# Kernel optimization log

Hardware: AMD Instinct MI355X
Metric: run time of the kernel (lower is better)

Reference implementation:

```python
import jax, jax.numpy as jnp
import numpy as np
import math

N, S, C, K, V = 32, 4096, 1, 512, 128
TARGET_SCALE = 0.06  # normalize_scale == embedding_scale when normalize=True


def setup_inputs() -> dict:
    key = jax.random.key(0)
    k1, k2 = jax.random.split(key)
    x0 = jax.random.normal(k1, (N, S, C, V), dtype=jnp.float32)
    emb = jax.random.normal(k2, (C, K, V), dtype=jnp.float32) * TARGET_SCALE
    # after_update(): renormalize each code vector to norm = embedding_scale*sqrt(V)
    tn = TARGET_SCALE * math.sqrt(V)
    emb = emb * (tn / jnp.linalg.norm(emb, axis=2, keepdims=True))
    return {"x0": x0, "embedding0": emb}


def _vq_forward(x0, embedding0):
    tn = TARGET_SCALE * math.sqrt(V)
    # normalize inputs and codebook to the same norm (normalize=True path)
    x = tn * x0 / jnp.linalg.norm(x0, axis=3, keepdims=True)              # (N,S,C,V)
    emb = tn * embedding0 / jnp.linalg.norm(embedding0, axis=2, keepdims=True)  # (C,K,V)

    xf = x.reshape(N * S, C, V)
    x2 = jnp.sum(xf * xf, axis=2)                     # (NS, C)
    e2 = jnp.sum(emb * emb, axis=2)                   # (C, K)
    dots = jnp.einsum('ncv,ckv->nck', xf, emb)        # (NS, C, K)
    d2 = x2[:, :, None] + e2[None, :, :] - 2.0 * dots
    index = jnp.argmin(d2, axis=2)                    # (NS, C) int

    # entropy of code usage: histc over n_classes, normalized by len(index)=NS
    hist = jnp.zeros((K,), jnp.float32).at[index.reshape(-1)].add(1.0)
    prob = hist / float(N * S)
    entropy = -jnp.sum(jnp.where(hist > 0, prob * jnp.log(jnp.where(hist > 0, prob, 1.0)), 0.0))

    # gather selected code vectors per channel
    output = emb[jnp.arange(C)[None, :], index]       # (NS, C, V)
    output = output.reshape(x.shape)                  # (N,S,C,V)

    sg = jax.lax.stop_gradient
    out0 = sg(output - x) + x                                              # straight-through
    out1 = jnp.sum((sg(x) - output) ** 2, axis=3)                          # codebook loss (N,S,C)
    out2 = jnp.sum((x - sg(output)) ** 2, axis=3) + jnp.sum((x - x0) ** 2, axis=3)  # commitment + norm penalty
    return out0, out1, out2, entropy


def reference(x0, embedding0):
    return _vq_forward(x0, embedding0)
```

## Files before the change

### kernel.cpp

```cpp
#include <hip/hip_runtime.h>
#include <math.h>

#define VDIM   128
#define KCODES 512
#define NROWS  (32 * 4096)
#define TILE_ROWS 512
#define NBLK (NROWS / TILE_ROWS)
#define TN 0.67882250993908565f

typedef __attribute__((ext_vector_type(8))) short bf16x8;
typedef __attribute__((ext_vector_type(4))) float f32x4;

__device__ __forceinline__ unsigned short f2bf(float f) {
    unsigned u = __float_as_uint(f);
    unsigned r = u + 0x7FFFu + ((u >> 16) & 1u);
    return (unsigned short)(r >> 16);
}

__device__ __forceinline__ bf16x8 pack8(f32x4 a, f32x4 b) {
    bf16x8 v;
    v[0] = (short)f2bf(a[0]); v[1] = (short)f2bf(a[1]);
    v[2] = (short)f2bf(a[2]); v[3] = (short)f2bf(a[3]);
    v[4] = (short)f2bf(b[0]); v[5] = (short)f2bf(b[1]);
    v[6] = (short)f2bf(b[2]); v[7] = (short)f2bf(b[3]);
    return v;
}

__global__ __launch_bounds__(1024, 1) void vq_fused(
        const float* __restrict__ x0,
        const float* __restrict__ emb0,
        unsigned short* __restrict__ hist_part,
        float* __restrict__ out0,
        float* __restrict__ out1,
        float* __restrict__ out2) {
    __shared__ uint4 sB[8192];
    __shared__ float sscale[KCODES];
    __shared__ int   shist[KCODES];
    __shared__ int   sbesti[TILE_ROWS];

    int t = threadIdx.x;
    int w = t >> 6;
    int l = t & 63;
    int n15 = l & 15;
    int q = l >> 4;

    int rowbase = blockIdx.x * TILE_ROWS + (w << 5);

    f32x4 ax[2][4][2];
    #pragma unroll
    for (int s = 0; s < 2; ++s) {
        const float* xrow = x0 + (size_t)(rowbase + (s << 4) + n15) * VDIM + (q << 3);
        #pragma unroll
        for (int kc = 0; kc < 4; ++kc) {
            const f32x4* xp = (const f32x4*)(xrow + (kc << 5));
            ax[s][kc][0] = xp[0];
            ax[s][kc][1] = xp[1];
        }
    }
    __builtin_amdgcn_sched_barrier(0);

    if (t < KCODES) shist[t] = 0;

    #pragma unroll 4
    for (int i = 0; i < 32; ++i) {
        int k = (w << 5) + i;
        const float* row = emb0 + (size_t)k * VDIM;
        float a = row[l];
        float b = row[l + 64];
        float ss = a * a + b * b;
        #pragma unroll
        for (int off = 32; off; off >>= 1) ss += __shfl_xor(ss, off);
        if (l == 0) sscale[k] = TN / sqrtf(ss);
    }

    __syncthreads();

    #pragma unroll
    for (int i = 0; i < 8; ++i) {
        int g = (i << 10) + t;
        int k = ((g >> 8) << 4) | (g & 15);
        int d0 = ((g >> 4) & 15) << 3;
        float s = sscale[k];
        const f32x4* ep = (const f32x4*)(emb0 + (size_t)k * VDIM + d0);
        f32x4 a = ep[0], b = ep[1];
        f32x4 as, bs;
        as[0] = a[0] * s; as[1] = a[1] * s; as[2] = a[2] * s; as[3] = a[3] * s;
        bs[0] = b[0] * s; bs[1] = b[1] * s; bs[2] = b[2] * s; bs[3] = b[3] * s;
        ((bf16x8*)sB)[g] = pack8(as, bs);
    }

    bf16x8 afr[2][4];
    float nsq[2];
    #pragma unroll
    for (int s = 0; s < 2; ++s) {
        float p0 = 0.f, p1 = 0.f;
        #pragma unroll
        for (int kc = 0; kc < 4; ++kc) {
            f32x4 a = ax[s][kc][0], b = ax[s][kc][1];
            p0 = fmaf(a[0], a[0], p0); p1 = fmaf(a[1], a[1], p1);
            p0 = fmaf(a[2], a[2], p0); p1 = fmaf(a[3], a[3], p1);
            p0 = fmaf(b[0], b[0], p0); p1 = fmaf(b[1], b[1], p1);
            p0 = fmaf(b[2], b[2], p0); p1 = fmaf(b[3], b[3], p1);
            afr[s][kc] = pack8(a, b);
        }
        nsq[s] = p0 + p1;
        nsq[s] += __shfl_xor(nsq[s], 16, 64);
        nsq[s] += __shfl_xor(nsq[s], 32, 64);
    }

    float best[2][4];
    int   bidx[2][4];
    #pragma unroll
    for (int s = 0; s < 2; ++s)
        #pragma unroll
        for (int r = 0; r < 4; ++r) { best[s][r] = -3.4e38f; bidx[s][r] = 0; }

    const f32x4 zero4 = {0.f, 0.f, 0.f, 0.f};

    __syncthreads();

    #pragma unroll 2
    for (int cn = 0; cn < 32; ++cn) {
        const bf16x8* bls = ((const bf16x8*)sB) + (cn << 8) + l;
        bf16x8 b0 = bls[0], b1 = bls[64], b2 = bls[128], b3 = bls[192];
        int nbase = (cn << 4) + n15;
        #pragma unroll
        for (int s = 0; s < 2; ++s) {
            f32x4 acc = __builtin_amdgcn_mfma_f32_16x16x32_bf16(afr[s][0], b0, zero4, 0, 0, 0);
            acc = __builtin_amdgcn_mfma_f32_16x16x32_bf16(afr[s][1], b1, acc, 0, 0, 0);
            acc = __builtin_amdgcn_mfma_f32_16x16x32_bf16(afr[s][2], b2, acc, 0, 0, 0);
            acc = __builtin_amdgcn_mfma_f32_16x16x32_bf16(afr[s][3], b3, acc, 0, 0, 0);
            #pragma unroll
            for (int r = 0; r < 4; ++r) {
                float d = acc[r];
                if (d > best[s][r]) { best[s][r] = d; bidx[s][r] = nbase; }
            }
        }
    }

    #pragma unroll
    for (int m = 1; m <= 8; m <<= 1) {
        #pragma unroll
        for (int s = 0; s < 2; ++s)
            #pragma unroll
            for (int r = 0; r < 4; ++r) {
                float ov = __shfl_xor(best[s][r], m, 64);
                int   oi = __shfl_xor(bidx[s][r], m, 64);
                if (ov > best[s][r] || (ov == best[s][r] && oi < bidx[s][r])) {
                    best[s][r] = ov; bidx[s][r] = oi;
                }
            }
    }

    int r3 = l & 3;
    bool own = (((l & 15) >> 2) == q);
    if (own) {
        #pragma unroll
        for (int s = 0; s < 2; ++s) {
            int rl = (s << 4) + (l & 15);
            size_t row = (size_t)rowbase + rl;
            float dv = best[s][r3];
            int   bv = bidx[s][r3];
            float nn = nsq[s];
            float sc = TN / sqrtf(nn);
            float o1 = 2.f * TN * TN - 2.f * sc * dv;
            __builtin_nontemporal_store(o1, &out1[row]);
            float sm = sc - 1.f;
            __builtin_nontemporal_store(o1 + sm * sm * nn, &out2[row]);
            atomicAdd(&shist[bv], 1);
            sbesti[(w << 5) + rl] = bv;
        }
    }

    #pragma unroll 4
    for (int p = 0; p < 16; ++p) {
        int rl = (p << 1) + (l >> 5);
        int bi = sbesti[(w << 5) + rl];
        float s = sscale[bi];
        int v4 = l & 31;
        f32x4 e = *((const f32x4*)(emb0 + (size_t)bi * VDIM) + v4);
        f32x4 o;
        o[0] = e[0] * s; o[1] = e[1] * s; o[2] = e[2] * s; o[3] = e[3] * s;
        __builtin_nontemporal_store(
            o, (f32x4*)(out0 + ((size_t)rowbase + rl) * (size_t)VDIM) + v4);
    }

    __syncthreads();

    if (t < KCODES)
        hist_part[((size_t)blockIdx.x << 9) + t] = (unsigned short)shist[t];
}

__global__ __launch_bounds__(1024) void entropy_k(
        const unsigned short* __restrict__ hp,
        float* __restrict__ out) {
    __shared__ int   s2[1024];
    __shared__ float red[8];
    int t = threadIdx.x;
    int c = t & 511;
    int half = t >> 9;
    int sum = 0;
    #pragma unroll 8
    for (int b = half * 128; b < half * 128 + 128; ++b)
        sum += hp[(b << 9) + c];
    s2[t] = sum;
    __syncthreads();
    if (t < 512) {
        float h = (float)(s2[t] + s2[t + 512]);
        float p = h / (float)NROWS;
        float term = (h > 0.f) ? p * logf(p) : 0.f;
        #pragma unroll
        for (int off = 32; off; off >>= 1) term += __shfl_xor(term, off);
        if ((t & 63) == 0) red[t >> 6] = term;
    }
    __syncthreads();
    if (t == 0) {
        float ssum = 0.f;
        #pragma unroll
        for (int i = 0; i < 8; i++) ssum += red[i];
        out[0] = -ssum;
    }
}

extern "C" void kernel_launch(void* const* d_in, const int* in_sizes, int n_in,
                              void* d_out, int out_size, void* d_ws, size_t ws_size,
                              hipStream_t stream) {
    const float* x0   = (const float*)d_in[0];
    const float* emb0 = (const float*)d_in[1];

    unsigned short* hist_part = (unsigned short*)d_ws;

    float* out  = (float*)d_out;
    float* out0 = out;
    float* out1 = out0 + (size_t)NROWS * VDIM;
    float* out2 = out1 + NROWS;
    float* oent = out2 + NROWS;

    vq_fused<<<NBLK, 1024, 0, stream>>>(x0, emb0, hist_part, out0, out1, out2);
    entropy_k<<<1, 1024, 0, stream>>>(hist_part, oent);
}
```

Before: 157.8 us.

## Halve row tile, stage codebook in two halves, use global atomic histogram

```diff
diff --git a/kernel.cpp b/kernel.cpp
--- a/kernel.cpp
+++ b/kernel.cpp
@@ -4,8 +4,9 @@
 #define VDIM   128
 #define KCODES 512
 #define NROWS  (32 * 4096)
-#define TILE_ROWS 512
+#define TILE_ROWS 256
 #define NBLK (NROWS / TILE_ROWS)
+#define STAGE_CODES 256
 #define TN 0.67882250993908565f
 
 typedef __attribute__((ext_vector_type(8))) short bf16x8;
@@ -26,14 +27,14 @@
     return v;
 }
 
-__global__ __launch_bounds__(1024, 1) void vq_fused(
+__global__ __launch_bounds__(1024, 8) void vq_fused(
         const float* __restrict__ x0,
         const float* __restrict__ emb0,
-        unsigned short* __restrict__ hist_part,
+        unsigned* __restrict__ hist,
         float* __restrict__ out0,
         float* __restrict__ out1,
         float* __restrict__ out2) {
-    __shared__ uint4 sB[8192];
+    __shared__ uint4 sB[4096];
     __shared__ float sscale[KCODES];
     __shared__ int   shist[KCODES];
     __shared__ int   sbesti[TILE_ROWS];
@@ -44,20 +45,18 @@
     int n15 = l & 15;
     int q = l >> 4;
 
-    int rowbase = blockIdx.x * TILE_ROWS + (w << 5);
-
-    f32x4 ax[2][4][2];
-    #pragma unroll
-    for (int s = 0; s < 2; ++s) {
-        const float* xrow = x0 + (size_t)(rowbase + (s << 4) + n15) * VDIM + (q << 3);
+    int rowbase = blockIdx.x * TILE_ROWS + (w << 4);
+
+    f32x4 ax[4][2];
+    {
+        const float* xrow = x0 + (size_t)(rowbase + n15) * VDIM + (q << 3);
         #pragma unroll
         for (int kc = 0; kc < 4; ++kc) {
             const f32x4* xp = (const f32x4*)(xrow + (kc << 5));
-            ax[s][kc][0] = xp[0];
-            ax[s][kc][1] = xp[1];
-        }
-    }
-    __builtin_amdgcn_sched_barrier(0);
+            ax[kc][0] = xp[0];
+            ax[kc][1] = xp[1];
+        }
+    }
 
     if (t < KCODES) shist[t] = 0;
 
@@ -75,65 +74,64 @@
 
     __syncthreads();
 
-    #pragma unroll
-    for (int i = 0; i < 8; ++i) {
-        int g = (i << 10) + t;
-        int k = ((g >> 8) << 4) | (g & 15);
-        int d0 = ((g >> 4) & 15) << 3;
-        float s = sscale[k];
-        const f32x4* ep = (const f32x4*)(emb0 + (size_t)k * VDIM + d0);
-        f32x4 a = ep[0], b = ep[1];
-        f32x4 as, bs;
-        as[0] = a[0] * s; as[1] = a[1] * s; as[2] = a[2] * s; as[3] = a[3] * s;
-        bs[0] = b[0] * s; bs[1] = b[1] * s; bs[2] = b[2] * s; bs[3] = b[3] * s;
-        ((bf16x8*)sB)[g] = pack8(as, bs);
-    }
-
-    bf16x8 afr[2][4];
-    float nsq[2];
-    #pragma unroll
-    for (int s = 0; s < 2; ++s) {
+    bf16x8 afr[4];
+    float nsq;
+    {
         float p0 = 0.f, p1 = 0.f;
         #pragma unroll
         for (int kc = 0; kc < 4; ++kc) {
-            f32x4 a = ax[s][kc][0], b = ax[s][kc][1];
+            f32x4 a = ax[kc][0], b = ax[kc][1];
             p0 = fmaf(a[0], a[0], p0); p1 = fmaf(a[1], a[1], p1);
             p0 = fmaf(a[2], a[2], p0); p1 = fmaf(a[3], a[3], p1);
             p0 = fmaf(b[0], b[0], p0); p1 = fmaf(b[1], b[1], p1);
             p0 = fmaf(b[2], b[2], p0); p1 = fmaf(b[3], b[3], p1);
-            afr[s][kc] = pack8(a, b);
-        }
-        nsq[s] = p0 + p1;
-        nsq[s] += __shfl_xor(nsq[s], 16, 64);
-        nsq[s] += __shfl_xor(nsq[s], 32, 64);
-    }
-
-    float best[2][4];
-    int   bidx[2][4];
+            afr[kc] = pack8(a, b);
+        }
+        nsq = p0 + p1;
+        nsq += __shfl_xor(nsq, 16, 64);
+        nsq += __shfl_xor(nsq, 32, 64);
+    }
+
+    float best[4];
+    int   bidx[4];
     #pragma unroll
-    for (int s = 0; s < 2; ++s)
-        #pragma unroll
-        for (int r = 0; r < 4; ++r) { best[s][r] = -3.4e38f; bidx[s][r] = 0; }
+    for (int r = 0; r < 4; ++r) { best[r] = -3.4e38f; bidx[r] = 0; }
 
     const f32x4 zero4 = {0.f, 0.f, 0.f, 0.f};
 
-    __syncthreads();
-
-    #pragma unroll 2
-    for (int cn = 0; cn < 32; ++cn) {
-        const bf16x8* bls = ((const bf16x8*)sB) + (cn << 8) + l;
-        bf16x8 b0 = bls[0], b1 = bls[64], b2 = bls[128], b3 = bls[192];
-        int nbase = (cn << 4) + n15;
-        #pragma unroll
-        for (int s = 0; s < 2; ++s) {
-            f32x4 acc = __builtin_amdgcn_mfma_f32_16x16x32_bf16(afr[s][0], b0, zero4, 0, 0, 0);
-            acc = __builtin_amdgcn_mfma_f32_16x16x32_bf16(afr[s][1], b1, acc, 0, 0, 0);
-            acc = __builtin_amdgcn_mfma_f32_16x16x32_bf16(afr[s][2], b2, acc, 0, 0, 0);
-            acc = __builtin_amdgcn_mfma_f32_16x16x32_bf16(afr[s][3], b3, acc, 0, 0, 0);
+    #pragma unroll 1
+    for (int st = 0; st < 2; ++st) {
+        if (st) __syncthreads();
+
+        int kofs = st << 8;
+        #pragma unroll
+        for (int i = 0; i < 4; ++i) {
+            int g = (i << 10) + t;
+            int k = kofs + (((g >> 8) << 4) | (g & 15));
+            int d0 = ((g >> 4) & 15) << 3;
+            float s = sscale[k];
+            const f32x4* ep = (const f32x4*)(emb0 + (size_t)k * VDIM + d0);
+            f32x4 a = ep[0], b = ep[1];
+            f32x4 as, bs;
+            as[0] = a[0] * s; as[1] = a[1] * s; as[2] = a[2] * s; as[3] = a[3] * s;
+            bs[0] = b[0] * s; bs[1] = b[1] * s; bs[2] = b[2] * s; bs[3] = b[3] * s;
+            ((bf16x8*)sB)[g] = pack8(as, bs);
+        }
+        __syncthreads();
+
+        #pragma unroll 2
+        for (int cn = 0; cn < 16; ++cn) {
+            const bf16x8* bls = ((const bf16x8*)sB) + (cn << 8) + l;
+            bf16x8 b0 = bls[0], b1 = bls[64], b2 = bls[128], b3 = bls[192];
+            int nbase = kofs + (cn << 4) + n15;
+            f32x4 acc = __builtin_amdgcn_mfma_f32_16x16x32_bf16(afr[0], b0, zero4, 0, 0, 0);
+            acc = __builtin_amdgcn_mfma_f32_16x16x32_bf16(afr[1], b1, acc, 0, 0, 0);
+            acc = __builtin_amdgcn_mfma_f32_16x16x32_bf16(afr[2], b2, acc, 0, 0, 0);
+            acc = __builtin_amdgcn_mfma_f32_16x16x32_bf16(afr[3], b3, acc, 0, 0, 0);
             #pragma unroll
             for (int r = 0; r < 4; ++r) {
                 float d = acc[r];
-                if (d > best[s][r]) { best[s][r] = d; bidx[s][r] = nbase; }
+                if (d > best[r]) { best[r] = d; bidx[r] = nbase; }
             }
         }
     }
@@ -141,41 +139,35 @@
     #pragma unroll
     for (int m = 1; m <= 8; m <<= 1) {
         #pragma unroll
-        for (int s = 0; s < 2; ++s)
-            #pragma unroll
-            for (int r = 0; r < 4; ++r) {
-                float ov = __shfl_xor(best[s][r], m, 64);
-                int   oi = __shfl_xor(bidx[s][r], m, 64);
-                if (ov > best[s][r] || (ov == best[s][r] && oi < bidx[s][r])) {
-                    best[s][r] = ov; bidx[s][r] = oi;
-                }
+        for (int r = 0; r < 4; ++r) {
+            float ov = __shfl_xor(best[r], m, 64);
+            int   oi = __shfl_xor(bidx[r], m, 64);
+            if (ov > best[r] || (ov == best[r] && oi < bidx[r])) {
+                best[r] = ov; bidx[r] = oi;
             }
+        }
     }
 
     int r3 = l & 3;
     bool own = (((l & 15) >> 2) == q);
     if (own) {
-        #pragma unroll
-        for (int s = 0; s < 2; ++s) {
-            int rl = (s << 4) + (l & 15);
-            size_t row = (size_t)rowbase + rl;
-            float dv = best[s][r3];
-            int   bv = bidx[s][r3];
-            float nn = nsq[s];
-            float sc = TN / sqrtf(nn);
-            float o1 = 2.f * TN * TN - 2.f * sc * dv;
-            __builtin_nontemporal_store(o1, &out1[row]);
-            float sm = sc - 1.f;
-            __builtin_nontemporal_store(o1 + sm * sm * nn, &out2[row]);
-            atomicAdd(&shist[bv], 1);
-            sbesti[(w << 5) + rl] = bv;
-        }
+        int rl = l & 15;
+        size_t row = (size_t)rowbase + rl;
+        float dv = best[r3];
+        int   bv = bidx[r3];
+        float sc = TN / sqrtf(nsq);
+        float o1 = 2.f * TN * TN - 2.f * sc * dv;
+        __builtin_nontemporal_store(o1, &out1[row]);
+        float sm = sc - 1.f;
+        __builtin_nontemporal_store(o1 + sm * sm * nsq, &out2[row]);
+        atomicAdd(&shist[bv], 1);
+        sbesti[(w << 4) + rl] = bv;
     }
 
     #pragma unroll 4
-    for (int p = 0; p < 16; ++p) {
+    for (int p = 0; p < 8; ++p) {
         int rl = (p << 1) + (l >> 5);
-        int bi = sbesti[(w << 5) + rl];
+        int bi = sbesti[(w << 4) + rl];
         float s = sscale[bi];
         int v4 = l & 31;
         f32x4 e = *((const f32x4*)(emb0 + (size_t)bi * VDIM) + v4);
@@ -187,32 +179,19 @@
 
     __syncthreads();
 
-    if (t < KCODES)
-        hist_part[((size_t)blockIdx.x << 9) + t] = (unsigned short)shist[t];
-}
-
-__global__ __launch_bounds__(1024) void entropy_k(
-        const unsigned short* __restrict__ hp,
-        float* __restrict__ out) {
-    __shared__ int   s2[1024];
+    if (t < KCODES && shist[t]) atomicAdd(&hist[t], (unsigned)shist[t]);
+}
+
+__global__ void entropy_k(const unsigned* __restrict__ hist,
+                          float* __restrict__ out) {
     __shared__ float red[8];
     int t = threadIdx.x;
-    int c = t & 511;
-    int half = t >> 9;
-    int sum = 0;
-    #pragma unroll 8
-    for (int b = half * 128; b < half * 128 + 128; ++b)
-        sum += hp[(b << 9) + c];
-    s2[t] = sum;
-    __syncthreads();
-    if (t < 512) {
-        float h = (float)(s2[t] + s2[t + 512]);
-        float p = h / (float)NROWS;
-        float term = (h > 0.f) ? p * logf(p) : 0.f;
-        #pragma unroll
-        for (int off = 32; off; off >>= 1) term += __shfl_xor(term, off);
-        if ((t & 63) == 0) red[t >> 6] = term;
-    }
+    float h = (float)hist[t];
+    float p = h / (float)NROWS;
+    float term = (h > 0.f) ? p * logf(p) : 0.f;
+    #pragma unroll
+    for (int off = 32; off; off >>= 1) term += __shfl_xor(term, off);
+    if ((t & 63) == 0) red[t >> 6] = term;
     __syncthreads();
     if (t == 0) {
         float ssum = 0.f;
@@ -228,7 +207,7 @@
     const float* x0   = (const float*)d_in[0];
     const float* emb0 = (const float*)d_in[1];
 
-    unsigned short* hist_part = (unsigned short*)d_ws;
+    unsigned* hist = (unsigned*)d_ws;
 
     float* out  = (float*)d_out;
     float* out0 = out;
@@ -236,6 +215,7 @@
     float* out2 = out1 + NROWS;
     float* oent = out2 + NROWS;
 
-    vq_fused<<<NBLK, 1024, 0, stream>>>(x0, emb0, hist_part, out0, out1, out2);
-    entropy_k<<<1, 1024, 0, stream>>>(hist_part, oent);
-}
+    hipMemsetAsync(hist, 0, KCODES * sizeof(unsigned), stream);
+    vq_fused<<<NBLK, 1024, 0, stream>>>(x0, emb0, hist, out0, out1, out2);
+    entropy_k<<<1, KCODES, 0, stream>>>(hist, oent);
+}
```

After: 164.7 us. +4.4%, slower.
